# Kernel optimization log

Hardware: AMD Instinct MI355X
Metric: run time of the kernel (lower is better)

## Reference

```python
import jax, jax.numpy as jnp
import numpy as np

EPS = 1e-5
K_GROUP = 8  # k_group_size


def setup_inputs() -> dict:
    key = jax.random.key(0)
    ks = jax.random.split(key, 8)
    C = 384  # encoder_channel
    rn = lambda k, s: (jax.random.normal(k, s, dtype=jnp.float32) * 0.05)
    return {
        "point_groups": jax.random.normal(ks[0], (4, 256, 32, 3), dtype=jnp.float32),
        # first_conv: Conv1d(3,128,1)+BN+ReLU+Conv1d(128,256,1)
        "W1": rn(ks[1], (128, 3)), "b1": jnp.zeros(128, jnp.float32),
        "gamma1": jnp.ones(128, jnp.float32), "beta1": jnp.zeros(128, jnp.float32),
        "W2": rn(ks[2], (256, 128)), "b2": jnp.zeros(256, jnp.float32),
        # second_conv: Conv1d(512,512,1)+BN+ReLU+Conv1d(512,C,1)
        "W3": rn(ks[3], (512, 512)), "b3": jnp.zeros(512, jnp.float32),
        "gamma3": jnp.ones(512, jnp.float32), "beta3": jnp.zeros(512, jnp.float32),
        "W4": rn(ks[4], (C, 512)), "b4": jnp.zeros(C, jnp.float32),
        # K_Norm affine (out_dim = C, matching declared parameter shapes)
        "alpha": jnp.ones((1, 1, 1, C), jnp.float32),
        "beta_aff": jnp.zeros((1, 1, 1, C), jnp.float32),
        # fusion_layer: Conv1d(2C,C,1)+BN+ReLU
        "Wf": rn(ks[5], (C, 2 * C)), "bf": jnp.zeros(C, jnp.float32),
        "gammaf": jnp.ones(C, jnp.float32), "betaf": jnp.zeros(C, jnp.float32),
    }


def _conv1x1(x, W, b):  # x: (B,Cin,L), W: (Cout,Cin)
    return jnp.einsum("bcl,oc->bol", x, W) + b[None, :, None]


def _bn(x, gamma, beta):  # training-mode BatchNorm1d over (batch, length)
    mu = jnp.mean(x, axis=(0, 2), keepdims=True)
    var = jnp.var(x, axis=(0, 2), keepdims=True)
    xh = (x - mu) * jax.lax.rsqrt(var + EPS)
    return xh * gamma[None, :, None] + beta[None, :, None]


def reference(point_groups, W1, b1, gamma1, beta1, W2, b2, W3, b3, gamma3, beta3,
              W4, b4, alpha, beta_aff, Wf, bf, gammaf, betaf):
    bs, g, n, _ = point_groups.shape
    C = W4.shape[0]
    pg = point_groups.reshape(bs * g, n, 3)  # (B', n, 3)

    # first_conv stack
    f = _conv1x1(pg.transpose(0, 2, 1), W1, b1)           # (B',128,n)
    f = jax.nn.relu(_bn(f, gamma1, beta1))
    f = _conv1x1(f, W2, b2)                               # (B',256,n)
    fg = jnp.max(f, axis=2, keepdims=True)                # (B',256,1)
    f = jnp.concatenate([jnp.broadcast_to(fg, f.shape), f], axis=1)  # (B',512,n)

    # second_conv stack
    f = _conv1x1(f, W3, b3)
    f = jax.nn.relu(_bn(f, gamma3, beta3))
    f = _conv1x1(f, W4, b4)                               # (B',C,n)
    feat = f.transpose(0, 2, 1)                           # (B',n,C)

    # KNN within each group (self included, as in KNN(xyz,xyz))
    sq = jnp.sum(pg * pg, axis=-1)                        # (B',n)
    d = sq[:, :, None] + sq[:, None, :] - 2.0 * jnp.einsum("bnc,bmc->bnm", pg, pg)
    _, idx = jax.lax.top_k(-d, K_GROUP)                   # (B',n,K)

    gather = jax.vmap(lambda a, i: a[i])
    knn_x = gather(feat, idx)                             # (B',n,K,C)

    # K_Norm: center-relative normalization by global scalar std (torch.std, ddof=1)
    mean_x = feat[:, :, None, :]
    dx = knn_x - mean_x
    std_x = jnp.std(dx, ddof=1)
    knn_x = dx / (std_x + EPS)
    knn_x = alpha * knn_x + beta_aff                      # (B',n,K,C)

    enhanced = jnp.mean(knn_x, axis=2)                    # mean over K -> (B',n,C)
    enhanced = jnp.mean(enhanced, axis=1)                 # pool over n -> (B',C)

    fg2 = jnp.max(f, axis=2)                              # (B',C)
    fused_in = jnp.concatenate([fg2, enhanced], axis=1)[:, :, None]  # (B',2C,1)
    fused = jax.nn.relu(_bn(_conv1x1(fused_in, Wf, bf), gammaf, betaf))[:, :, 0]
    return fused.reshape(bs, g, C)
```

## Files before the change

### kernel.cpp

```cpp
#include <hip/hip_runtime.h>
#include <math.h>

#define EPS 1e-5f

typedef __attribute__((ext_vector_type(8))) short s16x8;
typedef __attribute__((ext_vector_type(4))) float f32x4;

__device__ __forceinline__ unsigned short f2bf(float x) {
    unsigned u = __float_as_uint(x);
    u += 0x7fffu + ((u >> 16) & 1u);
    return (unsigned short)(u >> 16);
}
__device__ __forceinline__ float bf2f(unsigned short h) {
    return __uint_as_float(((unsigned)h) << 16);
}
__device__ __forceinline__ unsigned long long pack4bf(float a, float b, float c, float d) {
    return (unsigned long long)f2bf(a)
         | ((unsigned long long)f2bf(b) << 16)
         | ((unsigned long long)f2bf(c) << 32)
         | ((unsigned long long)f2bf(d) << 48);
}

template<int CTRL>
__device__ __forceinline__ float dppmov(float x) {
    return __int_as_float(__builtin_amdgcn_update_dpp(
        0, __float_as_int(x), CTRL, 0xF, 0xF, true));
}
__device__ __forceinline__ float red16_sum(float x) {
    x += dppmov<0xB1>(x);
    x += dppmov<0x4E>(x);
    x += dppmov<0x141>(x);
    x += dppmov<0x140>(x);
    return x;
}
__device__ __forceinline__ float red16_max(float x) {
    x = fmaxf(x, dppmov<0xB1>(x));
    x = fmaxf(x, dppmov<0x4E>(x));
    x = fmaxf(x, dppmov<0x141>(x));
    x = fmaxf(x, dppmov<0x140>(x));
    return x;
}

__global__ __launch_bounds__(128) void k1_conv1_knn(
    const float* __restrict__ pg, const float* __restrict__ W1,
    const float* __restrict__ b1,
    const float* __restrict__ W2, const float* __restrict__ W3,
    const float* __restrict__ W4, const float* __restrict__ Wf,
    unsigned short* __restrict__ h1b, float* __restrict__ p1s, float* __restrict__ p1q,
    int* __restrict__ idxw,
    unsigned short* __restrict__ W2b, unsigned short* __restrict__ W3b,
    unsigned short* __restrict__ W4b, unsigned short* __restrict__ Wfb)
{
    __shared__ float pgs[96];
    __shared__ float sqs[32];
    if (blockIdx.x >= 1024) {
        const int i = (blockIdx.x - 1024) * 128 + threadIdx.x;
        if (i < 32768)  W2b[i] = f2bf(W2[i]);
        if (i < 262144) W3b[i] = f2bf(W3[i]);
        if (i < 196608) W4b[i] = f2bf(W4[i]);
        if (i < 294912) Wfb[i] = f2bf(Wf[i]);
        return;
    }
    const int b = blockIdx.x;
    const int t = threadIdx.x;
    if (t < 96) pgs[t] = pg[b * 96 + t];
    __syncthreads();
    if (t < 32) {
        float x = pgs[t*3+0], y = pgs[t*3+1], z = pgs[t*3+2];
        sqs[t] = x*x + y*y + z*z;
    }
    __syncthreads();
    {
        const float w0 = W1[t*3+0], w1 = W1[t*3+1], w2 = W1[t*3+2];
        const float bb = b1[t];
        float s = 0.f, q = 0.f;
        unsigned short* hcol = h1b + (size_t)b*4096 + t;
        #pragma unroll
        for (int l = 0; l < 32; ++l) {
            float v = fmaf(w2, pgs[l*3+2], fmaf(w1, pgs[l*3+1], fmaf(w0, pgs[l*3+0], bb)));
            hcol[l*128] = f2bf(v); s += v; q += v*v;
        }
        p1s[b*128 + t] = s;
        p1q[b*128 + t] = q;
    }
    if (t < 32) {
        const float xl = pgs[t*3+0], yl = pgs[t*3+1], zl = pgs[t*3+2];
        const float sql = sqs[t];
        float dist[32];
        #pragma unroll
        for (int m = 0; m < 32; ++m) {
            float dot = xl*pgs[m*3+0] + yl*pgs[m*3+1] + zl*pgs[m*3+2];
            dist[m] = sql + sqs[m] - 2.f*dot;
        }
        unsigned used = 0u;
        int* orow = idxw + b*256 + t*8;
        #pragma unroll
        for (int j = 0; j < 8; ++j) {
            float best = 3.4e38f; int bi = 0;
            #pragma unroll
            for (int m = 0; m < 32; ++m) {
                if (!((used >> m) & 1u) && dist[m] < best) { best = dist[m]; bi = m; }
            }
            used |= (1u << bi);
            orow[j] = bi;
        }
    }
}

__global__ __launch_bounds__(256) void k_bn_fin2(
    const float* __restrict__ ps, const float* __restrict__ pq,
    int nPart, int nChan, float invN,
    const float* __restrict__ gamma, const float* __restrict__ beta,
    float* __restrict__ scale, float* __restrict__ shift)
{
    const int ob = blockIdx.x * 4;
    const int t = threadIdx.x;
    const int co = t & 3, i0 = t >> 2;
    float s = 0.f, q = 0.f;
    for (int i = i0; i < nPart; i += 64) {
        s += ps[(size_t)i*nChan + ob + co];
        q += pq[(size_t)i*nChan + ob + co];
    }
    #pragma unroll
    for (int off = 32; off >= 4; off >>= 1) {
        s += __shfl_down(s, off, 64);
        q += __shfl_down(q, off, 64);
    }
    __shared__ float ss[4][4], qs[4][4];
    const int wid = t >> 6, lane = t & 63;
    if (lane < 4) { ss[wid][lane] = s; qs[wid][lane] = q; }
    __syncthreads();
    if (t < 4) {
        float S = ss[0][t] + ss[1][t] + ss[2][t] + ss[3][t];
        float Q = qs[0][t] + qs[1][t] + qs[2][t] + qs[3][t];
        const int o = ob + t;
        float mu  = S * invN;
        float var = Q * invN - mu*mu;
        float sc  = gamma[o] * rsqrtf(var + EPS);
        scale[o] = sc;
        shift[o] = beta[o] - mu * sc;
    }
}

__global__ __launch_bounds__(512, 4) void k3_mfma(
    const unsigned short* __restrict__ h1b,
    const float* __restrict__ scale1, const float* __restrict__ shift1,
    const unsigned short* __restrict__ W2b, const float* __restrict__ b2,
    const unsigned short* __restrict__ W3b, const float* __restrict__ b3,
    unsigned short* __restrict__ h3b, float* __restrict__ p3s, float* __restrict__ p3q)
{
    const int g0 = blockIdx.x * 2;
    const int t = threadIdx.x;
    __shared__ __align__(16) unsigned short SB[17424];
    unsigned short* B1  = SB;
    unsigned short* F2  = SB;
    unsigned short* FGB = SB + 16896;

    {
        const int l = t >> 3, c0 = (t & 7) * 16;
        const int g = g0 + (l >> 5);
        #pragma unroll
        for (int h = 0; h < 2; ++h) {
            s16x8 hv = *(const s16x8*)(h1b + (size_t)g*4096 + (l & 31)*128 + c0 + h*8);
            unsigned short ov[8];
            #pragma unroll
            for (int e = 0; e < 8; ++e) {
                int c = c0 + h*8 + e;
                float v = fmaxf(fmaf(bf2f((unsigned short)hv[e]), scale1[c], shift1[c]), 0.f);
                ov[e] = f2bf(v);
            }
            uint4 o4;
            o4.x = (unsigned)ov[0] | ((unsigned)ov[1] << 16);
            o4.y = (unsigned)ov[2] | ((unsigned)ov[3] << 16);
            o4.z = (unsigned)ov[4] | ((unsigned)ov[5] << 16);
            o4.w = (unsigned)ov[6] | ((unsigned)ov[7] << 16);
            *(uint4*)&B1[l*136 + c0 + h*8] = o4;
        }
    }
    __syncthreads();

    const int wave = t >> 6;
    const int lane = t & 63;
    const int m    = lane & 15;
    const int quad = lane >> 4;

    f32x4 acc2[2][4];
    #pragma unroll
    for (int mt = 0; mt < 2; ++mt)
        #pragma unroll
        for (int n = 0; n < 4; ++n)
            acc2[mt][n] = (f32x4){0.f, 0.f, 0.f, 0.f};

    #pragma unroll
    for (int kt = 0; kt < 4; ++kt) {
        s16x8 bv[4];
        #pragma unroll
        for (int nt = 0; nt < 4; ++nt)
            bv[nt] = *(const s16x8*)&B1[(nt*16 + m)*136 + kt*32 + quad*8];
        #pragma unroll
        for (int mt = 0; mt < 2; ++mt) {
            s16x8 av = *(const s16x8*)(W2b + (size_t)(wave*32 + mt*16 + m)*128 + kt*32 + quad*8);
            #pragma unroll
            for (int nt = 0; nt < 4; ++nt)
                acc2[mt][nt] = __builtin_amdgcn_mfma_f32_16x16x32_bf16(av, bv[nt], acc2[mt][nt], 0, 0, 0);
        }
    }
    __syncthreads();

    #pragma unroll
    for (int mt = 0; mt < 2; ++mt) {
        const int o0 = wave*32 + mt*16 + quad*4;
        #pragma unroll
        for (int r = 0; r < 4; ++r) {
            float bb = b2[o0 + r];
            #pragma unroll
            for (int nt = 0; nt < 4; ++nt) acc2[mt][nt][r] += bb;
        }
        #pragma unroll
        for (int nt = 0; nt < 4; ++nt) {
            const int row = nt*16 + m;
            *(unsigned long long*)&F2[row*264 + o0] =
                pack4bf(acc2[mt][nt][0], acc2[mt][nt][1], acc2[mt][nt][2], acc2[mt][nt][3]);
        }
        float f0[4], f1[4];
        #pragma unroll
        for (int r = 0; r < 4; ++r) {
            f0[r] = red16_max(fmaxf(acc2[mt][0][r], acc2[mt][1][r]));
            f1[r] = red16_max(fmaxf(acc2[mt][2][r], acc2[mt][3][r]));
        }
        if (m == 0) {
            *(unsigned long long*)&FGB[o0]       = pack4bf(f0[0], f0[1], f0[2], f0[3]);
            *(unsigned long long*)&FGB[264 + o0] = pack4bf(f1[0], f1[1], f1[2], f1[3]);
        }
    }
    __syncthreads();

    f32x4 facc[4];
    #pragma unroll
    for (int i = 0; i < 4; ++i) facc[i] = (f32x4){0.f, 0.f, 0.f, 0.f};
    #pragma unroll
    for (int kt = 0; kt < 8; ++kt) {
        s16x8 bg = *(const s16x8*)&FGB[(m & 1)*264 + kt*32 + quad*8];
        #pragma unroll
        for (int i = 0; i < 4; ++i) {
            s16x8 av = *(const s16x8*)(W3b + (size_t)((wave*4 + i)*16 + m)*512 + kt*32 + quad*8);
            facc[i] = __builtin_amdgcn_mfma_f32_16x16x32_bf16(av, bg, facc[i], 0, 0, 0);
        }
    }

    f32x4 acc3[4][4];
    #pragma unroll
    for (int mt = 0; mt < 4; ++mt) {
        #pragma unroll
        for (int r = 0; r < 4; ++r) {
            const int ob = (wave*4 + mt)*16 + quad*4 + r;
            float self = facc[mt][r];
            float oth  = dppmov<0xB1>(self);
            float fg_g0 = (m & 1) ? oth : self;
            float fg_g1 = (m & 1) ? self : oth;
            float bb = b3[ob];
            acc3[mt][0][r] = bb + fg_g0;
            acc3[mt][1][r] = bb + fg_g0;
            acc3[mt][2][r] = bb + fg_g1;
            acc3[mt][3][r] = bb + fg_g1;
        }
    }
    #pragma unroll 4
    for (int kt = 0; kt < 8; ++kt) {
        s16x8 bv[4];
        #pragma unroll
        for (int nt = 0; nt < 4; ++nt)
            bv[nt] = *(const s16x8*)&F2[(nt*16 + m)*264 + kt*32 + quad*8];
        #pragma unroll
        for (int mt = 0; mt < 4; ++mt) {
            s16x8 av = *(const s16x8*)(W3b + (size_t)((wave*4 + mt)*16 + m)*512 + 256 + kt*32 + quad*8);
            #pragma unroll
            for (int nt = 0; nt < 4; ++nt)
                acc3[mt][nt] = __builtin_amdgcn_mfma_f32_16x16x32_bf16(av, bv[nt], acc3[mt][nt], 0, 0, 0);
        }
    }

    unsigned short* dst = h3b + (size_t)blockIdx.x * 32768;
    #pragma unroll
    for (int mt = 0; mt < 4; ++mt) {
        const int ot = wave*4 + mt;
        const int o0 = ot*16 + quad*4;
        float s[4], q[4];
        #pragma unroll
        for (int r = 0; r < 4; ++r) {
            float x0 = acc3[mt][0][r], x1 = acc3[mt][1][r];
            float x2 = acc3[mt][2][r], x3 = acc3[mt][3][r];
            s[r] = (x0 + x1) + (x2 + x3);
            q[r] = (x0*x0 + x1*x1) + (x2*x2 + x3*x3);
        }
        {
            unsigned long long u0 = pack4bf(acc3[mt][0][0], acc3[mt][0][1], acc3[mt][0][2], acc3[mt][0][3]);
            unsigned long long u1 = pack4bf(acc3[mt][1][0], acc3[mt][1][1], acc3[mt][1][2], acc3[mt][1][3]);
            unsigned long long u2 = pack4bf(acc3[mt][2][0], acc3[mt][2][1], acc3[mt][2][2], acc3[mt][2][3]);
            unsigned long long u3 = pack4bf(acc3[mt][3][0], acc3[mt][3][1], acc3[mt][3][2], acc3[mt][3][3]);
            unsigned short* p = dst + (size_t)(ot*64 + lane) * 16;
            *(uint4*)(p)     = make_uint4((unsigned)u0, (unsigned)(u0 >> 32), (unsigned)u1, (unsigned)(u1 >> 32));
            *(uint4*)(p + 8) = make_uint4((unsigned)u2, (unsigned)(u2 >> 32), (unsigned)u3, (unsigned)(u3 >> 32));
        }
        #pragma unroll
        for (int r = 0; r < 4; ++r) {
            s[r] = red16_sum(s[r]);
            q[r] = red16_sum(q[r]);
        }
        if (m == 0) {
            #pragma unroll
            for (int r = 0; r < 4; ++r) {
                p3s[(size_t)blockIdx.x*512 + o0 + r] = s[r];
                p3q[(size_t)blockIdx.x*512 + o0 + r] = q[r];
            }
        }
    }
}

__global__ __launch_bounds__(512, 4) void k5_mfma(
    const unsigned short* __restrict__ h3b,
    const float* __restrict__ scale3, const float* __restrict__ shift3,
    const unsigned short* __restrict__ W4b, const float* __restrict__ b4,
    const int* __restrict__ idxw,
    float* __restrict__ fg2, float* __restrict__ A,
    float* __restrict__ S1p, float* __restrict__ S2p)
{
    const int g0 = blockIdx.x * 2;
    const int t = threadIdx.x;
    __shared__ __align__(16) unsigned short SB[33280];
    unsigned short* B4 = SB;
    unsigned short* XT = SB;
    unsigned short* Mm = SB + 30720;
    __shared__ int icnt[2][32];
    __shared__ float r1[2][8], r2[2][8];

    {
        const uint4* src = (const uint4*)(h3b + (size_t)blockIdx.x * 32768);
        for (int i = t; i < 4096; i += 512) {
            uint4 hv = src[i];
            const int flat16 = i >> 1, half = i & 1;
            const int ln = flat16 & 63, m2 = ln & 15, q2 = ln >> 4;
            const int wm = flat16 >> 6;
            const int o0 = wm*16 + q2*4;
            const float4 sc = *(const float4*)(scale3 + o0);
            const float4 sh = *(const float4*)(shift3 + o0);
            const int rowa = (half*2)*16 + m2;
            float a0 = fmaxf(fmaf(bf2f((unsigned short)(hv.x       )), sc.x, sh.x), 0.f);
            float a1 = fmaxf(fmaf(bf2f((unsigned short)(hv.x >> 16 )), sc.y, sh.y), 0.f);
            float a2 = fmaxf(fmaf(bf2f((unsigned short)(hv.y       )), sc.z, sh.z), 0.f);
            float a3 = fmaxf(fmaf(bf2f((unsigned short)(hv.y >> 16 )), sc.w, sh.w), 0.f);
            float b0 = fmaxf(fmaf(bf2f((unsigned short)(hv.z       )), sc.x, sh.x), 0.f);
            float b1 = fmaxf(fmaf(bf2f((unsigned short)(hv.z >> 16 )), sc.y, sh.y), 0.f);
            float b2 = fmaxf(fmaf(bf2f((unsigned short)(hv.w       )), sc.z, sh.z), 0.f);
            float b3 = fmaxf(fmaf(bf2f((unsigned short)(hv.w >> 16 )), sc.w, sh.w), 0.f);
            *(unsigned long long*)&B4[rowa*520 + o0]        = pack4bf(a0, a1, a2, a3);
            *(unsigned long long*)&B4[(rowa + 16)*520 + o0] = pack4bf(b0, b1, b2, b3);
        }
    }
    if (t < 64) icnt[t >> 5][t & 31] = 0;
    __syncthreads();

    const int wave = t >> 6;
    const int lane = t & 63;
    const int m    = lane & 15;
    const int quad = lane >> 4;

    f32x4 acc4[3][4];
    #pragma unroll
    for (int mt = 0; mt < 3; ++mt)
        #pragma unroll
        for (int n = 0; n < 4; ++n)
            acc4[mt][n] = (f32x4){0.f, 0.f, 0.f, 0.f};

    #pragma unroll 4
    for (int kt = 0; kt < 16; ++kt) {
        s16x8 bv[4];
        #pragma unroll
        for (int nt = 0; nt < 4; ++nt)
            bv[nt] = *(const s16x8*)&B4[(nt*16 + m)*520 + kt*32 + quad*8];
        #pragma unroll
        for (int mt = 0; mt < 3; ++mt) {
            s16x8 av = *(const s16x8*)(W4b + (size_t)(wave*48 + mt*16 + m)*512 + kt*32 + quad*8);
            #pragma unroll
            for (int nt = 0; nt < 4; ++nt)
                acc4[mt][nt] = __builtin_amdgcn_mfma_f32_16x16x32_bf16(av, bv[nt], acc4[mt][nt], 0, 0, 0);
        }
    }

    #pragma unroll
    for (int mt = 0; mt < 3; ++mt) {
        const int o0 = wave*48 + mt*16 + quad*4;
        float f0[4], f1[4];
        #pragma unroll
        for (int r = 0; r < 4; ++r) {
            float bb = b4[o0 + r];
            #pragma unroll
            for (int nt = 0; nt < 4; ++nt) acc4[mt][nt][r] += bb;
            f0[r] = red16_max(fmaxf(acc4[mt][0][r], acc4[mt][1][r]));
            f1[r] = red16_max(fmaxf(acc4[mt][2][r], acc4[mt][3][r]));
        }
        if (m == 0) {
            #pragma unroll
            for (int r = 0; r < 4; ++r) {
                fg2[(size_t)g0*384 + o0 + r]     = f0[r];
                fg2[(size_t)(g0+1)*384 + o0 + r] = f1[r];
            }
        }
    }
    __syncthreads();

    #pragma unroll
    for (int mt = 0; mt < 3; ++mt) {
        const int o0 = wave*48 + mt*16 + quad*4;
        #pragma unroll
        for (int nt = 0; nt < 4; ++nt) {
            const int g = nt >> 1;
            const int l = (nt & 1)*16 + m;
            unsigned short* xg = XT + g*15360;
            #pragma unroll
            for (int r = 0; r < 4; ++r)
                xg[(o0 + r)*40 + l] = f2bf(acc4[mt][nt][r]);
        }
    }
    if (t < 64) {
        const int g = t >> 5, l = t & 31;
        uint4 z = make_uint4(0u, 0u, 0u, 0u);
        #pragma unroll
        for (int i = 0; i < 5; ++i)
            *(uint4*)&Mm[g*1280 + l*40 + i*8] = z;
    }
    __syncthreads();

    if (t < 64) {
        const int g = t >> 5, l = t & 31;
        const int* ip = idxw + (size_t)(g0 + g)*256 + l*8;
        #pragma unroll
        for (int j = 0; j < 8; ++j) {
            int ix = ip[j];
            Mm[g*1280 + l*40 + ix] = 0x3F80;
            atomicAdd(&icnt[g][ix], 1);
        }
    }
    __syncthreads();

    float s1loc[2] = {0.f, 0.f}, s2loc[2] = {0.f, 0.f};
    #pragma unroll
    for (int g = 0; g < 2; ++g) {
        const float c0 = (float)icnt[g][m];
        const float c1 = (float)icnt[g][m + 16];
        const float w0 = c0 - 8.f, u0 = c0 + 8.f;
        const float w1 = c1 - 8.f, u1 = c1 + 8.f;
        #pragma unroll
        for (int mt = 0; mt < 3; ++mt) {
            const int o0 = wave*48 + mt*16 + quad*4;
            float Ap[4];
            #pragma unroll
            for (int r = 0; r < 4; ++r) {
                const float x0 = acc4[mt][g*2 + 0][r];
                const float x1 = acc4[mt][g*2 + 1][r];
                Ap[r] = w0*x0 + w1*x1;
                s1loc[g] += Ap[r];
                s2loc[g] += u0*x0*x0 + u1*x1*x1;
            }
            #pragma unroll
            for (int r = 0; r < 4; ++r)
                Ap[r] = red16_sum(Ap[r]);
            if (m == 0) {
                #pragma unroll
                for (int r = 0; r < 4; ++r)
                    A[(size_t)(g0 + g)*384 + o0 + r] = Ap[r];
            }
        }
    }

    #pragma unroll
    for (int g = 0; g < 2; ++g) {
        const unsigned short* xg = XT + g*15360;
        float cross = 0.f;
        #pragma unroll
        for (int lt = 0; lt < 2; ++lt) {
            s16x8 af = *(const s16x8*)&Mm[g*1280 + (lt*16 + m)*40 + quad*8];
            #pragma unroll
            for (int i = 0; i < 3; ++i) {
                const int oc = (wave*3 + i)*16 + m;
                s16x8 bfv = *(const s16x8*)&xg[oc*40 + quad*8];
                f32x4 sa = __builtin_amdgcn_mfma_f32_16x16x32_bf16(
                    af, bfv, (f32x4){0.f, 0.f, 0.f, 0.f}, 0, 0, 0);
                #pragma unroll
                for (int r = 0; r < 4; ++r) {
                    const int lp = lt*16 + quad*4 + r;
                    cross = fmaf(bf2f(xg[oc*40 + lp]), sa[r], cross);
                }
            }
        }
        s2loc[g] -= 2.f * cross;
    }

    #pragma unroll
    for (int g = 0; g < 2; ++g) {
        float sA = s1loc[g], sQ = s2loc[g];
        #pragma unroll
        for (int off = 32; off > 0; off >>= 1) {
            sA += __shfl_down(sA, off, 64);
            sQ += __shfl_down(sQ, off, 64);
        }
        if (lane == 0) { r1[g][wave] = sA; r2[g][wave] = sQ; }
    }
    __syncthreads();
    if (t < 2) {
        float S = 0.f, Q = 0.f;
        #pragma unroll
        for (int w = 0; w < 8; ++w) { S += r1[t][w]; Q += r2[t][w]; }
        S1p[g0 + t] = S;
        S2p[g0 + t] = Q;
    }
}

__global__ __launch_bounds__(384) void k7_fused(
    const float* __restrict__ fg2, const float* __restrict__ A,
    const float* __restrict__ alpha, const float* __restrict__ beta_aff,
    const float* __restrict__ S1p, const float* __restrict__ S2p,
    const unsigned short* __restrict__ Wfb, const float* __restrict__ bf,
    float* __restrict__ hf, float* __restrict__ pfs, float* __restrict__ pfq)
{
    const int blk = blockIdx.x;
    const int g0 = blk * 16;
    const int t = threadIdx.x;
    __shared__ __align__(16) char smem[24832];
    unsigned short* xfb = (unsigned short*)smem;
    float* OTf = (float*)smem;
    __shared__ double rs[6], rq[6];
    __shared__ float stdsh;

    {
        double s = 0.0, q = 0.0;
        for (int i = t; i < 1024; i += 384) { s += (double)S1p[i]; q += (double)S2p[i]; }
        #pragma unroll
        for (int off = 32; off > 0; off >>= 1) {
            s += __shfl_down(s, off, 64);
            q += __shfl_down(q, off, 64);
        }
        if ((t & 63) == 0) { rs[t >> 6] = s; rq[t >> 6] = q; }
        __syncthreads();
        if (t == 0) {
            double S = 0.0, Q = 0.0;
            #pragma unroll
            for (int w = 0; w < 6; ++w) { S += rs[w]; Q += rq[w]; }
            const double N = 1024.0 * 32.0 * 8.0 * 384.0;
            double var = (Q - S*S/N) / (N - 1.0);
            stdsh = (float)sqrt(var);
        }
        __syncthreads();
    }
    const float inv = 1.f / (256.f * (stdsh + EPS));

    for (int i = t; i < 16*96; i += 384) {
        const int row = i / 96, c8 = (i % 96) * 8;
        const int g = g0 + row;
        float e[8];
        if (c8 < 384) {
            const float4* s0 = (const float4*)(fg2 + (size_t)g*384 + c8);
            float4 v0 = s0[0], v1 = s0[1];
            e[0]=v0.x; e[1]=v0.y; e[2]=v0.z; e[3]=v0.w;
            e[4]=v1.x; e[5]=v1.y; e[6]=v1.z; e[7]=v1.w;
        } else {
            const int cc = c8 - 384;
            const float4* s0 = (const float4*)(A + (size_t)g*384 + cc);
            float4 v0 = s0[0], v1 = s0[1];
            float av[8] = {v0.x,v0.y,v0.z,v0.w,v1.x,v1.y,v1.z,v1.w};
            #pragma unroll
            for (int j = 0; j < 8; ++j)
                e[j] = fmaf(alpha[cc+j] * inv, av[j], beta_aff[cc+j]);
        }
        uint4 o4;
        o4.x = (unsigned)f2bf(e[0]) | ((unsigned)f2bf(e[1]) << 16);
        o4.y = (unsigned)f2bf(e[2]) | ((unsigned)f2bf(e[3]) << 16);
        o4.z = (unsigned)f2bf(e[4]) | ((unsigned)f2bf(e[5]) << 16);
        o4.w = (unsigned)f2bf(e[6]) | ((unsigned)f2bf(e[7]) << 16);
        *(uint4*)&xfb[row*776 + c8] = o4;
    }
    __syncthreads();

    const int wave = t >> 6;
    const int lane = t & 63;
    const int m    = lane & 15;
    const int quad = lane >> 4;

    f32x4 acc[4];
    #pragma unroll
    for (int mt = 0; mt < 4; ++mt) acc[mt] = (f32x4){0.f, 0.f, 0.f, 0.f};

    #pragma unroll 4
    for (int kt = 0; kt < 24; ++kt) {
        s16x8 bv = *(const s16x8*)&xfb[m*776 + kt*32 + quad*8];
        #pragma unroll
        for (int mt = 0; mt < 4; ++mt) {
            s16x8 av = *(const s16x8*)(Wfb + (size_t)(wave*64 + mt*16 + m)*768 + kt*32 + quad*8);
            acc[mt] = __builtin_amdgcn_mfma_f32_16x16x32_bf16(av, bv, acc[mt], 0, 0, 0);
        }
    }

    #pragma unroll
    for (int mt = 0; mt < 4; ++mt) {
        const int o0 = wave*64 + mt*16 + quad*4;
        float s[4], q[4];
        #pragma unroll
        for (int r = 0; r < 4; ++r) {
            acc[mt][r] += bf[o0 + r];
            s[r] = red16_sum(acc[mt][r]);
            q[r] = red16_sum(acc[mt][r]*acc[mt][r]);
        }
        if (m == 0) {
            #pragma unroll
            for (int r = 0; r < 4; ++r) {
                pfs[(size_t)blk*384 + o0 + r] = s[r];
                pfq[(size_t)blk*384 + o0 + r] = q[r];
            }
        }
    }
    __syncthreads();

    #pragma unroll
    for (int mt = 0; mt < 4; ++mt) {
        const int o0 = wave*64 + mt*16 + quad*4;
        #pragma unroll
        for (int r = 0; r < 4; ++r)
            OTf[m*388 + o0 + r] = acc[mt][r];
    }
    __syncthreads();

    {
        float* dst = hf + (size_t)g0*384;
        #pragma unroll
        for (int k = 0; k < 4; ++k) {
            const int i = t + k*384;
            const int row = i / 96;
            float4 v = *(const float4*)&OTf[i*4 + row*4];
            *(float4*)(dst + i*4) = v;
        }
    }
}

__global__ __launch_bounds__(384) void k9_out(
    const float* __restrict__ hf,
    const float* __restrict__ pfs, const float* __restrict__ pfq,
    const float* __restrict__ gammaf, const float* __restrict__ betaf,
    float* __restrict__ out)
{
    const int blk = blockIdx.x, t = threadIdx.x;
    float S = 0.f, Q = 0.f;
    #pragma unroll 8
    for (int i = 0; i < 64; ++i) {
        S += pfs[(size_t)i*384 + t];
        Q += pfq[(size_t)i*384 + t];
    }
    const float mu  = S * (1.f/1024.f);
    const float var = Q * (1.f/1024.f) - mu*mu;
    const float sc  = gammaf[t] * rsqrtf(var + EPS);
    const float sh  = betaf[t] - mu * sc;
    const size_t base = (size_t)blk * 8 * 384;
    #pragma unroll
    for (int g = 0; g < 8; ++g) {
        float v = fmaf(hf[base + g*384 + t], sc, sh);
        out[base + g*384 + t] = fmaxf(v, 0.f);
    }
}

extern "C" void kernel_launch(void* const* d_in, const int* in_sizes, int n_in,
                              void* d_out, int out_size, void* d_ws, size_t ws_size,
                              hipStream_t stream) {
    const float* pg      = (const float*)d_in[0];
    const float* W1      = (const float*)d_in[1];
    const float* b1      = (const float*)d_in[2];
    const float* gamma1  = (const float*)d_in[3];
    const float* beta1   = (const float*)d_in[4];
    const float* W2      = (const float*)d_in[5];
    const float* b2      = (const float*)d_in[6];
    const float* W3      = (const float*)d_in[7];
    const float* b3      = (const float*)d_in[8];
    const float* gamma3  = (const float*)d_in[9];
    const float* beta3   = (const float*)d_in[10];
    const float* W4      = (const float*)d_in[11];
    const float* b4      = (const float*)d_in[12];
    const float* alpha   = (const float*)d_in[13];
    const float* beta_af = (const float*)d_in[14];
    const float* Wf      = (const float*)d_in[15];
    const float* bf      = (const float*)d_in[16];
    const float* gammaf  = (const float*)d_in[17];
    const float* betaf   = (const float*)d_in[18];
    float* out = (float*)d_out;

    float* w = (float*)d_ws;
    unsigned short* h1b = (unsigned short*)w; w += 1024*4096/2;
    unsigned short* h3b = (unsigned short*)w; w += 1024*16384/2;
    unsigned short* W2b = (unsigned short*)w; w += 32768/2;
    unsigned short* W3b = (unsigned short*)w; w += 262144/2;
    unsigned short* W4b = (unsigned short*)w; w += 196608/2;
    unsigned short* Wfb = (unsigned short*)w; w += 294912/2;
    float* hf     = w;  w += 1024*384;
    float* fg2    = w;  w += 1024*384;
    float* A      = w;  w += 1024*384;
    float* p1s    = w;  w += 1024*128;
    float* p1q    = w;  w += 1024*128;
    float* p3s    = w;  w += 1024*512;
    float* p3q    = w;  w += 1024*512;
    float* pfs    = w;  w += 64*384;
    float* pfq    = w;  w += 64*384;
    float* S1p    = w;  w += 1024;
    float* S2p    = w;  w += 1024;
    float* scale1 = w;  w += 128;
    float* shift1 = w;  w += 128;
    float* scale3 = w;  w += 512;
    float* shift3 = w;  w += 512;
    int*   idxw   = (int*)w;  w += 1024*256;

    hipLaunchKernelGGL(k1_conv1_knn, dim3(1024 + 2304), dim3(128), 0, stream,
                       pg, W1, b1, W2, W3, W4, Wf,
                       h1b, p1s, p1q, idxw, W2b, W3b, W4b, Wfb);
    hipLaunchKernelGGL(k_bn_fin2, dim3(32), dim3(256), 0, stream,
                       p1s, p1q, 1024, 128, 1.f/32768.f, gamma1, beta1, scale1, shift1);
    hipLaunchKernelGGL(k3_mfma, dim3(512), dim3(512), 0, stream,
                       h1b, scale1, shift1, W2b, b2, W3b, b3, h3b, p3s, p3q);
    hipLaunchKernelGGL(k_bn_fin2, dim3(128), dim3(256), 0, stream,
                       p3s, p3q, 512, 512, 1.f/32768.f, gamma3, beta3, scale3, shift3);
    hipLaunchKernelGGL(k5_mfma, dim3(512), dim3(512), 0, stream,
                       h3b, scale3, shift3, W4b, b4, idxw, fg2, A, S1p, S2p);
    hipLaunchKernelGGL(k7_fused, dim3(64), dim3(384), 0, stream,
                       fg2, A, alpha, beta_af, S1p, S2p, Wfb, bf, hf, pfs, pfq);
    hipLaunchKernelGGL(k9_out, dim3(128), dim3(384), 0, stream,
                       hf, pfs, pfq, gammaf, betaf, out);
}
```

Measured before the change: 219.5 us.

## Split fusion-layer GEMM output channels across four blocks per group slice

The fusion kernel now launches four blocks per 16-group slice, and each block computes 96 of the 384 output channels with one MFMA accumulator per wave. This raises the block count from 64 to 256 so more compute units share the small GEMM. In exchange, every block repeats the global std reduction and the construction of the bf16 input tile.

```diff
diff --git a/kernel.cpp b/kernel.cpp
--- a/kernel.cpp
+++ b/kernel.cpp
@@ -523,8 +523,11 @@
     const unsigned short* __restrict__ Wfb, const float* __restrict__ bf,
     float* __restrict__ hf, float* __restrict__ pfs, float* __restrict__ pfq)
 {
-    const int blk = blockIdx.x;
-    const int g0 = blk * 16;
+    const int blk    = blockIdx.x;
+    const int slice  = blk >> 2;
+    const int msplit = blk & 3;
+    const int g0     = slice * 16;
+    const int obase  = msplit * 96;
     const int t = threadIdx.x;
     __shared__ __align__(16) char smem[24832];
     unsigned short* xfb = (unsigned short*)smem;
@@ -586,58 +589,45 @@
     const int m    = lane & 15;
     const int quad = lane >> 4;
 
-    f32x4 acc[4];
-    #pragma unroll
-    for (int mt = 0; mt < 4; ++mt) acc[mt] = (f32x4){0.f, 0.f, 0.f, 0.f};
-
+    f32x4 acc = (f32x4){0.f, 0.f, 0.f, 0.f};
     #pragma unroll 4
     for (int kt = 0; kt < 24; ++kt) {
         s16x8 bv = *(const s16x8*)&xfb[m*776 + kt*32 + quad*8];
-        #pragma unroll
-        for (int mt = 0; mt < 4; ++mt) {
-            s16x8 av = *(const s16x8*)(Wfb + (size_t)(wave*64 + mt*16 + m)*768 + kt*32 + quad*8);
-            acc[mt] = __builtin_amdgcn_mfma_f32_16x16x32_bf16(av, bv, acc[mt], 0, 0, 0);
-        }
-    }
-
-    #pragma unroll
-    for (int mt = 0; mt < 4; ++mt) {
-        const int o0 = wave*64 + mt*16 + quad*4;
+        s16x8 av = *(const s16x8*)(Wfb + (size_t)(obase + wave*16 + m)*768 + kt*32 + quad*8);
+        acc = __builtin_amdgcn_mfma_f32_16x16x32_bf16(av, bv, acc, 0, 0, 0);
+    }
+
+    {
+        const int o0 = obase + wave*16 + quad*4;
         float s[4], q[4];
         #pragma unroll
         for (int r = 0; r < 4; ++r) {
-            acc[mt][r] += bf[o0 + r];
-            s[r] = red16_sum(acc[mt][r]);
-            q[r] = red16_sum(acc[mt][r]*acc[mt][r]);
+            acc[r] += bf[o0 + r];
+            s[r] = red16_sum(acc[r]);
+            q[r] = red16_sum(acc[r]*acc[r]);
         }
         if (m == 0) {
             #pragma unroll
             for (int r = 0; r < 4; ++r) {
-                pfs[(size_t)blk*384 + o0 + r] = s[r];
-                pfq[(size_t)blk*384 + o0 + r] = q[r];
+                pfs[(size_t)slice*384 + o0 + r] = s[r];
+                pfq[(size_t)slice*384 + o0 + r] = q[r];
             }
         }
     }
     __syncthreads();
 
-    #pragma unroll
-    for (int mt = 0; mt < 4; ++mt) {
-        const int o0 = wave*64 + mt*16 + quad*4;
+    {
+        const int lo0 = wave*16 + quad*4;
         #pragma unroll
         for (int r = 0; r < 4; ++r)
-            OTf[m*388 + o0 + r] = acc[mt][r];
+            OTf[m*100 + lo0 + r] = acc[r];
     }
     __syncthreads();
 
     {
-        float* dst = hf + (size_t)g0*384;
-        #pragma unroll
-        for (int k = 0; k < 4; ++k) {
-            const int i = t + k*384;
-            const int row = i / 96;
-            float4 v = *(const float4*)&OTf[i*4 + row*4];
-            *(float4*)(dst + i*4) = v;
-        }
+        const int grp = t / 24, c4 = t % 24;
+        float4 v = *(const float4*)&OTf[grp*100 + c4*4];
+        *(float4*)(hf + (size_t)(g0 + grp)*384 + obase + c4*4) = v;
     }
 }
 
@@ -725,7 +715,7 @@
                        p3s, p3q, 512, 512, 1.f/32768.f, gamma3, beta3, scale3, shift3);
     hipLaunchKernelGGL(k5_mfma, dim3(512), dim3(512), 0, stream,
                        h3b, scale3, shift3, W4b, b4, idxw, fg2, A, S1p, S2p);
-    hipLaunchKernelGGL(k7_fused, dim3(64), dim3(384), 0, stream,
+    hipLaunchKernelGGL(k7_fused, dim3(256), dim3(384), 0, stream,
                        fg2, A, alpha, beta_af, S1p, S2p, Wfb, bf, hf, pfs, pfq);
     hipLaunchKernelGGL(k9_out, dim3(128), dim3(384), 0, stream,
                        hf, pfs, pfq, gammaf, betaf, out);
```

After: 205.3 us. 1.07x faster.
